# Kernel optimization log

Measured on AMD Instinct MI355X. Metric: run time of the kernel, lower is better.

The kernel has to match this reference:

```python
import jax, jax.numpy as jnp
import numpy as np

EMBED_DIM = 1024
NUM_HEADS = 16
HEAD_DIM = EMBED_DIM // NUM_HEADS
WINDOW = 128  # window_size: attend to [i-W, i+W]


def setup_inputs() -> dict:
    key = jax.random.key(0)
    ks = jax.random.split(key, 9)
    B, S, E = 4, 4096, EMBED_DIM
    s = 1.0 / np.sqrt(E)
    return {
        "x": jax.random.normal(ks[0], (B, S, E), jnp.float32),
        "Wq": jax.random.normal(ks[1], (E, E), jnp.float32) * s,
        "bq": jnp.zeros((E,), jnp.float32),
        "Wk": jax.random.normal(ks[2], (E, E), jnp.float32) * s,
        "bk": jnp.zeros((E,), jnp.float32),
        "Wv": jax.random.normal(ks[3], (E, E), jnp.float32) * s,
        "bv": jnp.zeros((E,), jnp.float32),
        "Wo": jax.random.normal(ks[4], (E, E), jnp.float32) * s,
        "bo": jnp.zeros((E,), jnp.float32),
    }


def reference(x, Wq, bq, Wk, bk, Wv, bv, Wo, bo):
    B, S, E = x.shape
    H, D, W = NUM_HEADS, HEAD_DIM, WINDOW
    scale = jnp.sqrt(jnp.asarray(D, x.dtype))

    def heads(t):  # [B,S,E] -> [B,H,S,D]
        return t.reshape(B, S, H, D).transpose(0, 2, 1, 3)

    q = heads(x @ Wq + bq)
    k = heads(x @ Wk + bk)
    v = heads(x @ Wv + bv)

    # window indices per query position: j = i + [-W..W], masked to [0, S)
    offs = jnp.arange(-W, W + 1)                 # [2W+1]
    idx = jnp.arange(S)[:, None] + offs[None, :]  # [S, 2W+1]
    valid = (idx >= 0) & (idx < S)
    idxc = jnp.clip(idx, 0, S - 1)

    k_win = k[:, :, idxc, :]  # [B,H,S,2W+1,D]
    v_win = v[:, :, idxc, :]

    scores = jnp.einsum('bhsd,bhswd->bhsw', q, k_win) / scale
    scores = jnp.where(valid[None, None], scores, jnp.asarray(-jnp.inf, scores.dtype))
    attn = jax.nn.softmax(scores, axis=-1)
    out = jnp.einsum('bhsw,bhswd->bhsd', attn, v_win)  # [B,H,S,D]

    out = out.transpose(0, 2, 1, 3).reshape(B, S, E)
    return out @ Wo + bo
```

## Files before the change

kernel.cpp:

```cpp
#include <hip/hip_runtime.h>
#include <hip/hip_bf16.h>
#include <type_traits>

typedef unsigned short u16;
typedef __attribute__((ext_vector_type(8))) short  s16x8;
typedef __attribute__((ext_vector_type(8))) __bf16 b16x8;
typedef __attribute__((ext_vector_type(4))) float  f32x4;

#define S_LEN 4096
#define NB    4
#define EMB   1024
#define NH    16
#define HD    64
#define NROWS (NB * S_LEN)
#define KDIM  1024

static __device__ __forceinline__ u16 f2b(float f) {
  __hip_bfloat16 h = __float2bfloat16(f);
  return __builtin_bit_cast(u16, h);
}

template <typename T, typename = void>
struct mfma_takes : std::false_type {};
template <typename T>
struct mfma_takes<T, std::void_t<decltype(__builtin_amdgcn_mfma_f32_16x16x32_bf16(
    std::declval<T>(), std::declval<T>(), std::declval<f32x4>(), 0, 0, 0))>> : std::true_type {};

template <typename AB>
static __device__ __forceinline__ f32x4 mfma_any(AB a, AB b, f32x4 c) {
  return __builtin_amdgcn_mfma_f32_16x16x32_bf16(a, b, c, 0, 0, 0);
}

template <typename S8 = s16x8, typename B8 = b16x8>
static __device__ __forceinline__ f32x4 MFMA_BF16(s16x8 a, s16x8 b, f32x4 c) {
  if constexpr (mfma_takes<S8>::value)
    return mfma_any<S8>(__builtin_bit_cast(S8, a), __builtin_bit_cast(S8, b), c);
  else
    return mfma_any<B8>(__builtin_bit_cast(B8, a), __builtin_bit_cast(B8, b), c);
}

static __device__ __forceinline__ void gld_lds16(const void* g, void* l) {
  __builtin_amdgcn_global_load_lds((const __attribute__((address_space(1))) void*)g,
                                   (__attribute__((address_space(3))) void*)l, 16, 0, 0);
}

__global__ __launch_bounds__(256) void cvt_x_kernel(const float* __restrict__ in,
                                                    u16* __restrict__ out) {
  long i = ((long)blockIdx.x * 256 + threadIdx.x) * 8;
  float4 a = *(const float4*)(in + i);
  float4 b = *(const float4*)(in + i + 4);
  s16x8 o;
  o[0] = (short)f2b(a.x); o[1] = (short)f2b(a.y); o[2] = (short)f2b(a.z); o[3] = (short)f2b(a.w);
  o[4] = (short)f2b(b.x); o[5] = (short)f2b(b.y); o[6] = (short)f2b(b.z); o[7] = (short)f2b(b.w);
  *(s16x8*)(out + i) = o;
}

__global__ __launch_bounds__(256) void transpose_cvt4_kernel(
    const float* __restrict__ W0, const float* __restrict__ W1,
    const float* __restrict__ W2, const float* __restrict__ W3,
    u16* __restrict__ D0, u16* __restrict__ D1, u16* __restrict__ D2, u16* __restrict__ D3) {
  __shared__ float tile[32][33];
  const float* W; u16* D;
  switch (blockIdx.z) {
    case 0:  W = W0; D = D0; break;
    case 1:  W = W1; D = D1; break;
    case 2:  W = W2; D = D2; break;
    default: W = W3; D = D3; break;
  }
  int n0 = blockIdx.x * 32, k0 = blockIdx.y * 32;
  int tx = threadIdx.x & 31, ty = threadIdx.x >> 5;
#pragma unroll
  for (int i = ty; i < 32; i += 8)
    tile[i][tx] = W[(long)(k0 + i) * EMB + n0 + tx];
  __syncthreads();
#pragma unroll
  for (int i = ty; i < 32; i += 8)
    D[(long)(n0 + i) * EMB + k0 + tx] = f2b(tile[tx][i]);
}

#define SA_(p,k) (((p)*2+(k))*8192)
#define SB_(p,k) (32768 + ((p)*2+(k))*8192)

__global__ __launch_bounds__(512, 2) void gemm8p_kernel(
    const u16* __restrict__ A, const u16* __restrict__ Bt,
    const float* __restrict__ b0, const float* __restrict__ b1, const float* __restrict__ b2,
    void* __restrict__ Cp, int N, int out_f32) {
  __shared__ __align__(16) u16 smem[65536];
  const int tid = threadIdx.x;
  const int w = tid >> 6, lane = tid & 63;
  const int wm = w >> 2, wn = w & 3;
  const int frow = lane & 15, fg = lane >> 4;

  const int nwg = gridDim.x;
  const int bid = ((int)blockIdx.x & 7) * (nwg >> 3) + ((int)blockIdx.x >> 3);
  const int nbn = N >> 8;
  const int bm = bid / nbn, bn = bid % nbn;

  int offA[8];
#pragma unroll
  for (int j = 0; j < 8; j++) {
    int row = wm * 128 + j * 16 + frow;
    offA[j] = row * 32 + ((fg ^ ((row ^ (row >> 2)) & 3)) << 3);
  }
  int offB[4];
#pragma unroll
  for (int j = 0; j < 4; j++) {
    int row = wn * 64 + j * 16 + frow;
    offB[j] = row * 32 + ((fg ^ ((row ^ (row >> 2)) & 3)) << 3);
  }
  int srow[2], soff[2];
#pragma unroll
  for (int L = 0; L < 2; L++) {
    int lin = L * 512 + tid;
    int r = lin >> 2;
    srow[L] = r;
    soff[L] = (((lin & 3) ^ ((r ^ (r >> 2)) & 3)) << 3);
  }
  const u16* Abase = A + (long)bm * 256 * KDIM;
  const u16* Bbase = Bt + (long)bn * 256 * KDIM;

  f32x4 acc[8][4];
#pragma unroll
  for (int m = 0; m < 8; m++)
#pragma unroll
    for (int n = 0; n < 4; n++) acc[m][n] = (f32x4)0.0f;

  auto STAGE = [&](const u16* gb, int kcol, int slot) {
#pragma unroll
    for (int L = 0; L < 2; L++)
      gld_lds16(gb + (long)srow[L] * KDIM + kcol + soff[L],
                &smem[slot + (L * 512 + w * 64) * 8]);
  };

  s16x8 af[4], bf[4];

  STAGE(Abase, 0,  SA_(0,0)); STAGE(Bbase, 0,  SB_(0,0));
  STAGE(Abase, 32, SA_(0,1)); STAGE(Bbase, 32, SB_(0,1));
  STAGE(Abase, 64, SA_(1,0)); STAGE(Bbase, 64, SB_(1,0));
  asm volatile("s_waitcnt vmcnt(8)" ::: "memory");
  asm volatile("s_barrier" ::: "memory");

#define PHASE(p, k, mh, RDB, GB, KCOL, SLOT, DOVM)                            \
  {                                                                           \
    if (RDB) {                                                                \
      _Pragma("unroll") for (int n = 0; n < 4; n++)                           \
        bf[n] = *(const s16x8*)&smem[SB_(p, k) + offB[n]];                    \
    }                                                                         \
    _Pragma("unroll") for (int m = 0; m < 4; m++)                             \
      af[m] = *(const s16x8*)&smem[SA_(p, k) + offA[(mh) * 4 + m]];           \
    STAGE(GB, KCOL, SLOT);                                                    \
    asm volatile("s_barrier" ::: "memory");                                   \
    asm volatile("s_waitcnt lgkmcnt(0)" ::: "memory");                        \
    __builtin_amdgcn_sched_barrier(0);                                        \
    __builtin_amdgcn_s_setprio(1);                                            \
    _Pragma("unroll") for (int m = 0; m < 4; m++)                             \
      _Pragma("unroll") for (int n = 0; n < 4; n++)                           \
        acc[(mh) * 4 + m][n] = MFMA_BF16(af[m], bf[n], acc[(mh) * 4 + m][n]); \
    __builtin_amdgcn_s_setprio(0);                                            \
    if (DOVM) asm volatile("s_waitcnt vmcnt(8)" ::: "memory");                \
    asm volatile("s_barrier" ::: "memory");                                   \
  }

#pragma unroll 1
  for (int i = 0; i < 8; i++) {
    const int t = 2 * i;
    const int k1 = ((t + 1) & 15) * 64;
    const int k2 = ((t + 2) & 15) * 64;
    const int k3 = ((t + 3) & 15) * 64;
    PHASE(0, 0, 0, 1, Abase, k1 + 32, SA_(1, 1), 0)
    PHASE(0, 0, 1, 0, Bbase, k1 + 32, SB_(1, 1), 1)
    PHASE(0, 1, 0, 1, Abase, k2,      SA_(0, 0), 0)
    PHASE(0, 1, 1, 0, Bbase, k2,      SB_(0, 0), 1)
    PHASE(1, 0, 0, 1, Abase, k2 + 32, SA_(0, 1), 0)
    PHASE(1, 0, 1, 0, Bbase, k2 + 32, SB_(0, 1), 1)
    PHASE(1, 1, 0, 1, Abase, k3,      SA_(1, 0), 0)
    PHASE(1, 1, 1, 0, Bbase, k3,      SB_(1, 0), 1)
  }
#undef PHASE

  asm volatile("s_waitcnt vmcnt(0)" ::: "memory");
  asm volatile("s_barrier" ::: "memory");

  const long crow0 = (long)(bm * 256) * N + bn * 256;
  if (!out_f32) {
    u16* buf = &smem[w * 4096];
#pragma unroll
    for (int mf = 0; mf < 8; mf++) {
#pragma unroll
      for (int n = 0; n < 4; n++) {
        int gc = bn * 256 + wn * 64 + n * 16 + frow;
        int which = gc >> 10;
        const float* bias = (which == 0) ? b0 : ((which == 1) ? b1 : b2);
        float bv = bias[gc & 1023];
#pragma unroll
        for (int r = 0; r < 4; r++)
          buf[(4 * fg + r) * 72 + n * 16 + frow] = f2b(acc[mf][n][r] + bv);
      }
      asm volatile("s_waitcnt lgkmcnt(0)" ::: "memory");
      __builtin_amdgcn_sched_barrier(0);
#pragma unroll
      for (int q = 0; q < 2; q++) {
        int row = q * 8 + (lane >> 3);
        int ch = lane & 7;
        s16x8 v = *(const s16x8*)&buf[row * 72 + ch * 8];
        long gr = (long)(wm * 128 + mf * 16 + row);
        *(s16x8*)((u16*)Cp + crow0 + gr * N + wn * 64 + ch * 8) = v;
      }
      asm volatile("s_waitcnt lgkmcnt(0)" ::: "memory");
      __builtin_amdgcn_sched_barrier(0);
    }
  } else {
    float* fbuf = (float*)&smem[w * 4096];
#pragma unroll
    for (int mf = 0; mf < 8; mf++) {
#pragma unroll
      for (int n = 0; n < 4; n++) {
        float bv = b0[(bn * 256 + wn * 64 + n * 16 + frow) & 1023];
#pragma unroll
        for (int r = 0; r < 4; r++)
          fbuf[(4 * fg + r) * 68 + n * 16 + frow] = acc[mf][n][r] + bv;
      }
      asm volatile("s_waitcnt lgkmcnt(0)" ::: "memory");
      __builtin_amdgcn_sched_barrier(0);
#pragma unroll
      for (int q = 0; q < 4; q++) {
        int row = q * 4 + (lane >> 4);
        int ch = lane & 15;
        float4 v = *(const float4*)&fbuf[row * 68 + ch * 4];
        long gr = (long)(wm * 128 + mf * 16 + row);
        *(float4*)((float*)Cp + crow0 + gr * N + wn * 64 + ch * 4) = v;
      }
      asm volatile("s_waitcnt lgkmcnt(0)" ::: "memory");
      __builtin_amdgcn_sched_barrier(0);
    }
  }
}

#define QBLK 128
#define LPITCH 72

__global__ __launch_bounds__(256) void attn_kernel(const u16* __restrict__ QKV,
                                                   u16* __restrict__ Oa) {
  __shared__ u16 lK[64 * LPITCH];
  __shared__ u16 lV[64 * LPITCH];
  __shared__ u16 lP[4 * 32 * LPITCH];

  const int tid = threadIdx.x;
  const int w = tid >> 6, lane = tid & 63;
  const int frow = lane & 15, fg = lane >> 4;

  const int nq = S_LEN / QBLK;
  const int bid = blockIdx.x;
  const int b = bid / (NH * nq);
  const int rem = bid % (NH * nq);
  const int h = rem / nq;
  const int qt = rem % nq;
  const int q0 = qt * QBLK;
  const int qw0 = q0 + 32 * w;

  const u16* base = QKV + (long)b * S_LEN * 3072 + h * 64;

  s16x8 qf[2][2];
#pragma unroll
  for (int m = 0; m < 2; m++)
#pragma unroll
    for (int kk = 0; kk < 2; kk++)
      qf[m][kk] = *(const s16x8*)(base + (long)(qw0 + 16 * m + frow) * 3072 + kk * 32 + 8 * fg);

  f32x4 acc[2][4];
#pragma unroll
  for (int m = 0; m < 2; m++)
#pragma unroll
    for (int n = 0; n < 4; n++) acc[m][n] = (f32x4)0.0f;
  float mrow[2][4], lrow[2][4];
#pragma unroll
  for (int m = 0; m < 2; m++)
#pragma unroll
    for (int rg = 0; rg < 4; rg++) { mrow[m][rg] = -1e30f; lrow[m][rg] = 0.f; }

  u16* lPw = &lP[w * 32 * LPITCH];

  for (int t = 0; t < 6; t++) {
    const int kvb = q0 - 128 + t * 64;
    if (kvb + 63 < 0 || kvb >= S_LEN) continue;
    {
      const int srow = tid >> 3;
      const int sc8 = tid & 7;
#pragma unroll
      for (int pass = 0; pass < 2; pass++) {
        int row = srow + pass * 32;
        int kv = kvb + row;
        s16x8 kd = (s16x8)0, vd = (s16x8)0;
        if (kv >= 0 && kv < S_LEN) {
          kd = *(const s16x8*)(base + 1024 + (long)kv * 3072 + sc8 * 8);
          vd = *(const s16x8*)(base + 2048 + (long)kv * 3072 + sc8 * 8);
        }
        *(s16x8*)&lK[row * LPITCH + sc8 * 8] = kd;
        const int swz = row ^ (sc8 << 3);
#pragma unroll
        for (int j = 0; j < 8; j++) lV[(sc8 * 8 + j) * LPITCH + swz] = (u16)vd[j];
      }
    }
    __syncthreads();
    const bool active = (kvb + 63 >= qw0 - 128) && (kvb <= qw0 + 159);
    if (active) {
      f32x4 sfr[2][4];
#pragma unroll
      for (int m = 0; m < 2; m++)
#pragma unroll
        for (int n = 0; n < 4; n++) sfr[m][n] = (f32x4)0.0f;
#pragma unroll
      for (int kk = 0; kk < 2; kk++) {
        s16x8 kb[4];
#pragma unroll
        for (int n = 0; n < 4; n++)
          kb[n] = *(const s16x8*)&lK[(16 * n + frow) * LPITCH + (fg + 4 * kk) * 8];
#pragma unroll
        for (int m = 0; m < 2; m++)
#pragma unroll
          for (int n = 0; n < 4; n++)
            sfr[m][n] = MFMA_BF16(qf[m][kk], kb[n], sfr[m][n]);
      }
#pragma unroll
      for (int m = 0; m < 2; m++) {
#pragma unroll
        for (int rg = 0; rg < 4; rg++) {
          const int q = qw0 + 16 * m + 4 * fg + rg;
          float sv[4];
          float smax = -1e30f;
#pragma unroll
          for (int n = 0; n < 4; n++) {
            int kv = kvb + 16 * n + frow;
            bool valid = (kv >= q - 128) && (kv <= q + 128) && (kv >= 0) && (kv < S_LEN);
            float xv = valid ? sfr[m][n][rg] * 0.125f : -1e30f;
            sv[n] = xv;
            smax = fmaxf(smax, xv);
          }
          smax = fmaxf(smax, __shfl_xor(smax, 1));
          smax = fmaxf(smax, __shfl_xor(smax, 2));
          smax = fmaxf(smax, __shfl_xor(smax, 4));
          smax = fmaxf(smax, __shfl_xor(smax, 8));
          float mold = mrow[m][rg];
          float mnew = fmaxf(mold, smax);
          float alpha = __expf(mold - mnew);
          mrow[m][rg] = mnew;
          float psum = 0.f;
#pragma unroll
          for (int n = 0; n < 4; n++) {
            float p = (sv[n] > -1e29f) ? __expf(sv[n] - mnew) : 0.f;
            psum += p;
            lPw[(16 * m + 4 * fg + rg) * LPITCH + 16 * n + frow] = f2b(p);
          }
          psum += __shfl_xor(psum, 1);
          psum += __shfl_xor(psum, 2);
          psum += __shfl_xor(psum, 4);
          psum += __shfl_xor(psum, 8);
          lrow[m][rg] = lrow[m][rg] * alpha + psum;
#pragma unroll
          for (int n = 0; n < 4; n++) acc[m][n][rg] *= alpha;
        }
      }
      __threadfence_block();
#pragma unroll
      for (int kt = 0; kt < 2; kt++) {
        s16x8 pa[2], vb[4];
#pragma unroll
        for (int m = 0; m < 2; m++)
          pa[m] = *(const s16x8*)&lPw[(16 * m + frow) * LPITCH + (fg + 4 * kt) * 8];
#pragma unroll
        for (int n = 0; n < 4; n++) {
          const int d = 16 * n + frow;
          const int key = (d >> 3) & 7;
          const int o = (fg + 4 * kt) ^ key;
          vb[n] = *(const s16x8*)&lV[d * LPITCH + o * 8];
        }
#pragma unroll
        for (int m = 0; m < 2; m++)
#pragma unroll
          for (int n = 0; n < 4; n++)
            acc[m][n] = MFMA_BF16(pa[m], vb[n], acc[m][n]);
      }
    }
    __syncthreads();
  }

#pragma unroll
  for (int m = 0; m < 2; m++)
#pragma unroll
    for (int rg = 0; rg < 4; rg++) {
      const float inv = 1.0f / lrow[m][rg];
#pragma unroll
      for (int n = 0; n < 4; n++)
        lPw[(16 * m + 4 * fg + rg) * LPITCH + 16 * n + frow] = f2b(acc[m][n][rg] * inv);
    }
  asm volatile("s_waitcnt lgkmcnt(0)" ::: "memory");
  u16* Ob = Oa + ((long)(b * S_LEN + qw0)) * EMB + h * HD;
#pragma unroll
  for (int i = 0; i < 4; i++) {
    int flat = lane + 64 * i;
    int row = flat >> 3, ch = flat & 7;
    *(s16x8*)(Ob + (long)row * EMB + ch * 8) = *(const s16x8*)&lPw[row * LPITCH + ch * 8];
  }
}

extern "C" void kernel_launch(void* const* d_in, const int* in_sizes, int n_in,
                              void* d_out, int out_size, void* d_ws, size_t ws_size,
                              hipStream_t stream) {
  const float* x  = (const float*)d_in[0];
  const float* Wq = (const float*)d_in[1];
  const float* bq = (const float*)d_in[2];
  const float* Wk = (const float*)d_in[3];
  const float* bk = (const float*)d_in[4];
  const float* Wv = (const float*)d_in[5];
  const float* bv = (const float*)d_in[6];
  const float* Wo = (const float*)d_in[7];
  const float* bo = (const float*)d_in[8];

  char* ws = (char*)d_ws;
  u16* xb   = (u16*)ws;  ws += (size_t)NROWS * EMB * 2;
  u16* Wt   = (u16*)ws;  ws += (size_t)3 * EMB * EMB * 2;
  u16* Wot  = (u16*)ws;  ws += (size_t)EMB * EMB * 2;
  u16* QKVb = (u16*)ws;  ws += (size_t)NROWS * 3 * EMB * 2;
  u16* Oab  = (u16*)ws;  ws += (size_t)NROWS * EMB * 2;

  cvt_x_kernel<<<(NROWS * EMB) / (256 * 8), 256, 0, stream>>>(x, xb);

  dim3 tg(EMB / 32, EMB / 32, 4);
  transpose_cvt4_kernel<<<tg, 256, 0, stream>>>(
      Wq, Wk, Wv, Wo, Wt, Wt + (size_t)EMB * EMB, Wt + (size_t)2 * EMB * EMB, Wot);

  gemm8p_kernel<<<(NROWS / 256) * (3 * EMB / 256), 512, 0, stream>>>(
      xb, Wt, bq, bk, bv, QKVb, 3 * EMB, 0);

  attn_kernel<<<NB * NH * (S_LEN / QBLK), 256, 0, stream>>>(QKVb, Oab);

  gemm8p_kernel<<<(NROWS / 256) * (EMB / 256), 512, 0, stream>>>(
      Oab, Wot, bo, bo, bo, d_out, EMB, 1);
}
```

Baseline: 288.5 us.

## Keep attention probabilities in registers via transposed QK^T MFMA, drop LDS P buffer

The score MFMA now takes its operands swapped so each lane holds scores for one query row. Softmax then reduces across only two cross-lane shuffles, and the probabilities are packed straight into the A operand of the PV MFMA. This removes the LDS round trip for P, the per-row 4-step shuffle reductions and the block fence. Other changes: the V fragments are read as two 4-wide LDS loads, the output staging reuses the K/V shared buffer, and block IDs are remapped in an 8-way interleave. The cost is extra shuffles to broadcast the rescale factors and more register pressure.

Result: faster. 260.1 us (-9.9%).

```diff
diff --git a/kernel.cpp b/kernel.cpp
--- a/kernel.cpp
+++ b/kernel.cpp
@@ -4,6 +4,7 @@
 
 typedef unsigned short u16;
 typedef __attribute__((ext_vector_type(8))) short  s16x8;
+typedef __attribute__((ext_vector_type(4))) short  s16x4;
 typedef __attribute__((ext_vector_type(8))) __bf16 b16x8;
 typedef __attribute__((ext_vector_type(4))) float  f32x4;
 
@@ -241,16 +242,17 @@
 
 __global__ __launch_bounds__(256) void attn_kernel(const u16* __restrict__ QKV,
                                                    u16* __restrict__ Oa) {
-  __shared__ u16 lK[64 * LPITCH];
-  __shared__ u16 lV[64 * LPITCH];
-  __shared__ u16 lP[4 * 32 * LPITCH];
+  __shared__ __align__(16) u16 smem[9216];
+  u16* lK = smem;
+  u16* lV = smem + 64 * LPITCH;
 
   const int tid = threadIdx.x;
   const int w = tid >> 6, lane = tid & 63;
   const int frow = lane & 15, fg = lane >> 4;
 
   const int nq = S_LEN / QBLK;
-  const int bid = blockIdx.x;
+  int bid = (int)blockIdx.x;
+  bid = (bid & 7) * ((NB * NH * nq) >> 3) + (bid >> 3);
   const int b = bid / (NH * nq);
   const int rem = bid % (NH * nq);
   const int h = rem / nq;
@@ -272,23 +274,18 @@
   for (int m = 0; m < 2; m++)
 #pragma unroll
     for (int n = 0; n < 4; n++) acc[m][n] = (f32x4)0.0f;
-  float mrow[2][4], lrow[2][4];
-#pragma unroll
-  for (int m = 0; m < 2; m++)
-#pragma unroll
-    for (int rg = 0; rg < 4; rg++) { mrow[m][rg] = -1e30f; lrow[m][rg] = 0.f; }
-
-  u16* lPw = &lP[w * 32 * LPITCH];
+  float mrow[2] = {-1e30f, -1e30f};
+  float lrow[2] = {0.f, 0.f};
 
   for (int t = 0; t < 6; t++) {
     const int kvb = q0 - 128 + t * 64;
     if (kvb + 63 < 0 || kvb >= S_LEN) continue;
     {
-      const int srow = tid >> 3;
+      const int srowt = tid >> 3;
       const int sc8 = tid & 7;
 #pragma unroll
       for (int pass = 0; pass < 2; pass++) {
-        int row = srow + pass * 32;
+        int row = srowt + pass * 32;
         int kv = kvb + row;
         s16x8 kd = (s16x8)0, vd = (s16x8)0;
         if (kv >= 0 && kv < S_LEN) {
@@ -319,87 +316,97 @@
         for (int m = 0; m < 2; m++)
 #pragma unroll
           for (int n = 0; n < 4; n++)
-            sfr[m][n] = MFMA_BF16(qf[m][kk], kb[n], sfr[m][n]);
+            sfr[m][n] = MFMA_BF16(kb[n], qf[m][kk], sfr[m][n]);
       }
 #pragma unroll
       for (int m = 0; m < 2; m++) {
-#pragma unroll
-        for (int rg = 0; rg < 4; rg++) {
-          const int q = qw0 + 16 * m + 4 * fg + rg;
-          float sv[4];
-          float smax = -1e30f;
-#pragma unroll
-          for (int n = 0; n < 4; n++) {
-            int kv = kvb + 16 * n + frow;
+        const int q = qw0 + 16 * m + frow;
+        float p[4][4];
+        float tmax = -1e30f;
+#pragma unroll
+        for (int n = 0; n < 4; n++)
+#pragma unroll
+          for (int r = 0; r < 4; r++) {
+            int kv = kvb + 16 * n + 4 * fg + r;
             bool valid = (kv >= q - 128) && (kv <= q + 128) && (kv >= 0) && (kv < S_LEN);
-            float xv = valid ? sfr[m][n][rg] * 0.125f : -1e30f;
-            sv[n] = xv;
-            smax = fmaxf(smax, xv);
+            float xv = valid ? sfr[m][n][r] * 0.125f : -1e30f;
+            p[n][r] = xv;
+            tmax = fmaxf(tmax, xv);
           }
-          smax = fmaxf(smax, __shfl_xor(smax, 1));
-          smax = fmaxf(smax, __shfl_xor(smax, 2));
-          smax = fmaxf(smax, __shfl_xor(smax, 4));
-          smax = fmaxf(smax, __shfl_xor(smax, 8));
-          float mold = mrow[m][rg];
-          float mnew = fmaxf(mold, smax);
-          float alpha = __expf(mold - mnew);
-          mrow[m][rg] = mnew;
-          float psum = 0.f;
-#pragma unroll
-          for (int n = 0; n < 4; n++) {
-            float p = (sv[n] > -1e29f) ? __expf(sv[n] - mnew) : 0.f;
-            psum += p;
-            lPw[(16 * m + 4 * fg + rg) * LPITCH + 16 * n + frow] = f2b(p);
+        tmax = fmaxf(tmax, __shfl_xor(tmax, 16));
+        tmax = fmaxf(tmax, __shfl_xor(tmax, 32));
+        float mold = mrow[m];
+        float mnew = fmaxf(mold, tmax);
+        float al = __expf(mold - mnew);
+        mrow[m] = mnew;
+        float ps = 0.f;
+#pragma unroll
+        for (int n = 0; n < 4; n++)
+#pragma unroll
+          for (int r = 0; r < 4; r++) {
+            float e = (p[n][r] > -1e29f) ? __expf(p[n][r] - mnew) : 0.f;
+            p[n][r] = e;
+            ps += e;
           }
-          psum += __shfl_xor(psum, 1);
-          psum += __shfl_xor(psum, 2);
-          psum += __shfl_xor(psum, 4);
-          psum += __shfl_xor(psum, 8);
-          lrow[m][rg] = lrow[m][rg] * alpha + psum;
-#pragma unroll
-          for (int n = 0; n < 4; n++) acc[m][n][rg] *= alpha;
+        ps += __shfl_xor(ps, 16);
+        ps += __shfl_xor(ps, 32);
+        lrow[m] = lrow[m] * al + ps;
+        float a4[4];
+#pragma unroll
+        for (int r = 0; r < 4; r++) a4[r] = __shfl(al, 20 * fg + r);
+#pragma unroll
+        for (int nd = 0; nd < 4; nd++)
+#pragma unroll
+          for (int r = 0; r < 4; r++) acc[m][nd][r] *= a4[r];
+#pragma unroll
+        for (int kt = 0; kt < 2; kt++) {
+          s16x8 pa;
+#pragma unroll
+          for (int j = 0; j < 8; j++)
+            pa[j] = (short)f2b(p[2 * kt + (j >> 2)][j & 3]);
+#pragma unroll
+          for (int nd = 0; nd < 4; nd++) {
+            const int d = 16 * nd + frow;
+            const int key = ((d >> 3) & 7) << 3;
+            const u16* vrow = &lV[d * LPITCH];
+            const int a0 = (32 * kt + 4 * fg) ^ key;
+            const int a1 = (32 * kt + 16 + 4 * fg) ^ key;
+            s16x4 lo = *(const s16x4*)&vrow[a0];
+            s16x4 hi = *(const s16x4*)&vrow[a1];
+            s16x8 vb;
+            vb[0] = lo[0]; vb[1] = lo[1]; vb[2] = lo[2]; vb[3] = lo[3];
+            vb[4] = hi[0]; vb[5] = hi[1]; vb[6] = hi[2]; vb[7] = hi[3];
+            acc[m][nd] = MFMA_BF16(pa, vb, acc[m][nd]);
+          }
         }
-      }
-      __threadfence_block();
-#pragma unroll
-      for (int kt = 0; kt < 2; kt++) {
-        s16x8 pa[2], vb[4];
-#pragma unroll
-        for (int m = 0; m < 2; m++)
-          pa[m] = *(const s16x8*)&lPw[(16 * m + frow) * LPITCH + (fg + 4 * kt) * 8];
-#pragma unroll
-        for (int n = 0; n < 4; n++) {
-          const int d = 16 * n + frow;
-          const int key = (d >> 3) & 7;
-          const int o = (fg + 4 * kt) ^ key;
-          vb[n] = *(const s16x8*)&lV[d * LPITCH + o * 8];
-        }
-#pragma unroll
-        for (int m = 0; m < 2; m++)
-#pragma unroll
-          for (int n = 0; n < 4; n++)
-            acc[m][n] = MFMA_BF16(pa[m], vb[n], acc[m][n]);
       }
     }
     __syncthreads();
   }
 
+  float i4[2][4];
+#pragma unroll
+  for (int m = 0; m < 2; m++) {
+    float inv = 1.0f / lrow[m];
+#pragma unroll
+    for (int r = 0; r < 4; r++) i4[m][r] = __shfl(inv, 20 * fg + r);
+  }
+  u16* bb = smem + w * 2304;
 #pragma unroll
   for (int m = 0; m < 2; m++)
 #pragma unroll
-    for (int rg = 0; rg < 4; rg++) {
-      const float inv = 1.0f / lrow[m][rg];
-#pragma unroll
-      for (int n = 0; n < 4; n++)
-        lPw[(16 * m + 4 * fg + rg) * LPITCH + 16 * n + frow] = f2b(acc[m][n][rg] * inv);
-    }
+    for (int nd = 0; nd < 4; nd++)
+#pragma unroll
+      for (int r = 0; r < 4; r++)
+        bb[(16 * m + 4 * fg + r) * LPITCH + 16 * nd + frow] = f2b(acc[m][nd][r] * i4[m][r]);
   asm volatile("s_waitcnt lgkmcnt(0)" ::: "memory");
+  __builtin_amdgcn_sched_barrier(0);
   u16* Ob = Oa + ((long)(b * S_LEN + qw0)) * EMB + h * HD;
 #pragma unroll
   for (int i = 0; i < 4; i++) {
     int flat = lane + 64 * i;
     int row = flat >> 3, ch = flat & 7;
-    *(s16x8*)(Ob + (long)row * EMB + ch * 8) = *(const s16x8*)&lPw[row * LPITCH + ch * 8];
+    *(s16x8*)(Ob + (long)row * EMB + ch * 8) = *(const s16x8*)&bb[row * LPITCH + ch * 8];
   }
 }
 
```
